# Kernel optimization log

Measured on AMD Instinct MI355X. Metric: run time of the kernel, lower is better.

## Reference

```python
import jax, jax.numpy as jnp
import numpy as np

DIM, IDIM, HEADS = 256, 64, 4
B, I, J = 1, 256, 256
EPS = 1e-5


def _sinu(seq, rot):
    inv = 1.0 / (10000.0 ** (np.arange(0, rot, 2, dtype=np.float64) / rot))
    f = np.arange(seq, dtype=np.float64)[:, None] * inv[None, :]   # [seq, rot/2]
    f = np.repeat(f, 2, axis=-1)                                   # [seq, rot]
    return (jnp.asarray(np.sin(f)[None], dtype=jnp.float32),
            jnp.asarray(np.cos(f)[None], dtype=jnp.float32))       # [1, seq, rot]


def setup_inputs() -> dict:
    key = jax.random.key(0)
    ks = jax.random.split(key, 8)
    w = DIM ** -0.5
    sin_i, cos_i = _sinu(J, IDIM)
    sin_j, cos_j = _sinu(I, IDIM)
    return {
        'x': jax.random.normal(ks[0], (B, I, J, DIM), jnp.float32),
        'sin_i': sin_i, 'cos_i': cos_i, 'sin_j': sin_j, 'cos_j': cos_j,
        'gia': jnp.ones((DIM,), jnp.float32), 'bia': jnp.zeros((DIM,), jnp.float32),
        'gib': jnp.ones((DIM,), jnp.float32), 'bib': jnp.zeros((DIM,), jnp.float32),
        'Wq_i': jax.random.normal(ks[1], (DIM, IDIM * HEADS), jnp.float32) * w,
        'Wkv_i': jax.random.normal(ks[2], (DIM, 2 * IDIM * HEADS), jnp.float32) * w,
        'Wo_i': jax.random.normal(ks[3], (IDIM * HEADS, DIM), jnp.float32) * w,
        'bo_i': jnp.zeros((DIM,), jnp.float32),
        'gja': jnp.ones((DIM,), jnp.float32), 'bja': jnp.zeros((DIM,), jnp.float32),
        'gjb': jnp.ones((DIM,), jnp.float32), 'bjb': jnp.zeros((DIM,), jnp.float32),
        'Wq_j': jax.random.normal(ks[4], (DIM, IDIM * HEADS), jnp.float32) * w,
        'Wkv_j': jax.random.normal(ks[5], (DIM, 2 * IDIM * HEADS), jnp.float32) * w,
        'Wo_j': jax.random.normal(ks[6], (IDIM * HEADS, DIM), jnp.float32) * w,
        'bo_j': jnp.zeros((DIM,), jnp.float32),
    }


def _ln(x, g, b):
    mu = jnp.mean(x, axis=-1, keepdims=True)
    var = jnp.mean((x - mu) ** 2, axis=-1, keepdims=True)
    return (x - mu) / jnp.sqrt(var + EPS) * g + b


def _rotate_every_two(x):
    x1, x2 = x[..., ::2], x[..., 1::2]
    return jnp.stack((-x2, x1), axis=-1).reshape(x.shape)


def _rope(x, sin, cos):
    # sin/cos: [1, seq, rot] -> [1, 1, seq, rot] (broadcast over heads)
    sin, cos = sin[:, None], cos[:, None]
    rd = sin.shape[-1]
    xr, xp = x[..., :rd], x[..., rd:]
    xr = xr * cos + _rotate_every_two(xr) * sin
    return jnp.concatenate((xr, xp), axis=-1)


def _attn(a, sin, cos, ga, ba, gb, bb, Wq, Wkv, Wo, bo):
    an = _ln(a, ga, ba)
    bn = _ln(a, gb, bb)  # a == b in axial use
    q = an @ Wq
    k, v = jnp.split(bn @ Wkv, 2, axis=-1)
    Bn, N = a.shape[0], a.shape[1]
    def heads(t):
        return t.reshape(Bn, N, HEADS, IDIM).transpose(0, 2, 1, 3)  # b h n d
    q, k, v = heads(q), heads(k), heads(v)
    q = _rope(q, sin, cos)
    k = _rope(k, sin, cos)
    dots = jnp.einsum('bhid,bhjd->bhij', q, k)  # scale = 1 (as in source)
    attn = jax.nn.softmax(dots, axis=-1)
    out = jnp.einsum('bhij,bhjd->bhid', attn, v)
    out = out.transpose(0, 2, 3, 1).reshape(Bn, N, IDIM * HEADS)  # 'b h i d -> b i (d h)'
    return jax.nn.elu(out @ Wo + bo)


def reference(x, sin_i, cos_i, sin_j, cos_j,
              gia, bia, gib, bib, Wq_i, Wkv_i, Wo_i, bo_i,
              gja, bja, gjb, bjb, Wq_j, Wkv_j, Wo_j, bo_j):
    b, i, j, d = x.shape
    xi = x.reshape(b * i, j, d)
    xi = _attn(xi, sin_i, cos_i, gia, bia, gib, bib, Wq_i, Wkv_i, Wo_i, bo_i)
    xi = xi.reshape(b, i, j, d)
    xj = x.transpose(0, 2, 1, 3).reshape(b * j, i, d)
    xj = _attn(xj, sin_j, cos_j, gja, bja, gjb, bjb, Wq_j, Wkv_j, Wo_j, bo_j)
    xj = xj.reshape(b, j, i, d).transpose(0, 2, 1, 3)
    return x + (xi + xj) / 2
```

## Files before the change

kernel.cpp:

```cpp
#include <hip/hip_runtime.h>
#include <math.h>

#define DIM    256
#define IDIM   64
#define HEADS  4
#define NSEQ   256
#define SEQLEN 256
#define NTOK   (NSEQ * SEQLEN)
#define EPSLN  1e-5f

typedef __attribute__((ext_vector_type(8))) short bf16x8s;
typedef __attribute__((ext_vector_type(4))) float f32x4;

union BF8 { bf16x8s v; unsigned short u[8]; };

__device__ __forceinline__ float bf2f(unsigned short u) {
    union { unsigned int i; float f; } v; v.i = ((unsigned int)u) << 16; return v.f;
}
__device__ __forceinline__ unsigned short f2bf(float f) {
    union { float f; unsigned int i; } v; v.f = f;
    unsigned int x = v.i;
    return (unsigned short)((x + 0x7fffu + ((x >> 16) & 1u)) >> 16);
}

__device__ bf16x8s g_wpk[8][8192];
__device__ float g_bias[8][256];
__device__ float g_csum[8][256];

__global__ __launch_bounds__(256) void wpack_all_kernel(
    const float* __restrict__ Wq_i, const float* __restrict__ Wkv_i,
    const float* __restrict__ Wo_i,
    const float* __restrict__ Wq_j, const float* __restrict__ Wkv_j,
    const float* __restrict__ Wo_j,
    const float* __restrict__ gia, const float* __restrict__ gib,
    const float* __restrict__ gja, const float* __restrict__ gjb)
{
    const int slot = blockIdx.y;
    const int pass = slot >> 2, m = slot & 3;
    const float* W; int ldw, col0, perm;
    const float* gam;
    if (m == 0)      { W = pass ? Wq_j  : Wq_i;  ldw = 256; col0 = 0;   perm = 0; gam = pass ? gja : gia; }
    else if (m == 1) { W = pass ? Wkv_j : Wkv_i; ldw = 512; col0 = 0;   perm = 0; gam = pass ? gjb : gib; }
    else if (m == 2) { W = pass ? Wkv_j : Wkv_i; ldw = 512; col0 = 256; perm = 0; gam = pass ? gjb : gib; }
    else             { W = pass ? Wo_j  : Wo_i;  ldw = 256; col0 = 0;   perm = 1; gam = 0; }

    const int gtile = blockIdx.x * 4 + (threadIdx.x >> 6);
    const int l = threadIdx.x & 63;
    const int nt = gtile >> 3, kt = gtile & 7;
    const int n = nt * 16 + (l & 15);
    const int k0 = kt * 32 + (l >> 4) * 8;
    BF8 o;
#pragma unroll
    for (int j = 0; j < 8; ++j) {
        int k = k0 + j;
        int src = perm ? ((k & 63) * 4 + (k >> 6)) : k;
        float wv = W[(size_t)src * ldw + col0 + n];
        if (gam) wv *= gam[k];
        o.u[j] = f2bf(wv);
    }
    g_wpk[slot][(size_t)gtile * 64 + l] = o.v;
}

__global__ __launch_bounds__(256) void bias_kernel(
    const float* __restrict__ bia, const float* __restrict__ bib,
    const float* __restrict__ bja, const float* __restrict__ bjb,
    const float* __restrict__ gia, const float* __restrict__ gib,
    const float* __restrict__ gja, const float* __restrict__ gjb,
    const float* __restrict__ Wq_i, const float* __restrict__ Wkv_i,
    const float* __restrict__ Wq_j, const float* __restrict__ Wkv_j)
{
    const int s = blockIdx.x;
    const int pass = s / 3, m = s % 3;
    const float* beta = (m == 0) ? (pass ? bja : bia) : (pass ? bjb : bib);
    const float* gam  = (m == 0) ? (pass ? gja : gia) : (pass ? gjb : gib);
    const float* W    = (m == 0) ? (pass ? Wq_j : Wq_i) : (pass ? Wkv_j : Wkv_i);
    const int ldw  = (m == 0) ? 256 : 512;
    const int col0 = (m == 2) ? 256 : 0;
    const int col  = threadIdx.x;
    float ab = 0.f, ac = 0.f;
    for (int k = 0; k < 256; ++k) {
        float wv = W[(size_t)k * ldw + col0 + col];
        ab += beta[k] * wv;
        ac += gam[k]  * wv;
    }
    g_bias[pass * 4 + m][col] = ab;
    g_csum[pass * 4 + m][col] = ac;
}

#define HLD  264
#define CLD2 261

__global__ __launch_bounds__(1024) void lnqkv_kernel(
    const float* __restrict__ x,
    const float* __restrict__ sin_t, const float* __restrict__ cos_t,
    bf16x8s* __restrict__ qo, bf16x8s* __restrict__ ko, bf16x8s* __restrict__ vo,
    int pass)
{
    __shared__ __align__(16) unsigned short smu[17024];
    unsigned short* hi = smu;
    unsigned short* lo = smu + 8448;
    float* stats = (float*)(smu + 16896);
    float* smf = (float*)smu;

    const int tid = threadIdx.x;
    const int l = tid & 63, w = tid >> 6;
    const int lr = l & 15, lk = l >> 4;
    const int t0 = blockIdx.x * 32;
    const int seq = t0 >> 8;
    const int pos0 = t0 & 255;
    const int wbase = pass * 4;

    {
        const int r  = tid >> 5;
        const int c0 = (tid & 31) * 8;
        int t = t0 + r;
        int row = (pass == 0) ? t : ((t & 255) * NSEQ + (t >> 8));
        const float4* xp = reinterpret_cast<const float4*>(&x[(size_t)row * DIM + c0]);
        float4 v0 = xp[0], v1 = xp[1];
        float vv[8] = {v0.x, v0.y, v0.z, v0.w, v1.x, v1.y, v1.z, v1.w};
        BF8 hh, ll;
#pragma unroll
        for (int j = 0; j < 8; ++j) {
            union { float f; unsigned int u; } a; a.f = vv[j];
            unsigned short h = (unsigned short)(a.u >> 16);
            hh.u[j] = h;
            ll.u[j] = f2bf(vv[j] - bf2f(h));
        }
        *reinterpret_cast<bf16x8s*>(hi + r * HLD + c0) = hh.v;
        *reinterpret_cast<bf16x8s*>(lo + r * HLD + c0) = ll.v;
    }
    __syncthreads();

    {
        const int r = tid >> 5, sub = tid & 31;
        BF8 h0, l0;
        h0.v = *(const bf16x8s*)(hi + r * HLD + sub * 8);
        l0.v = *(const bf16x8s*)(lo + r * HLD + sub * 8);
        float s1 = 0.f, s2 = 0.f;
#pragma unroll
        for (int m = 0; m < 8; ++m) {
            float v = bf2f(h0.u[m]) + bf2f(l0.u[m]);
            s1 += v; s2 += v * v;
        }
        for (int off = 1; off < 32; off <<= 1) {
            s1 += __shfl_xor(s1, off, 32);
            s2 += __shfl_xor(s2, off, 32);
        }
        float mu = s1 * (1.f / 256.f);
        float var = s2 * (1.f / 256.f) - mu * mu;
        float rstd = rsqrtf(var + EPSLN);
        if (sub == 0) { stats[r] = rstd; stats[32 + r] = mu * rstd; }
    }
    __syncthreads();

    f32x4 acc[2][3];
#pragma unroll
    for (int mp2 = 0; mp2 < 2; ++mp2)
#pragma unroll
        for (int nf = 0; nf < 3; ++nf) { f32x4 z = {0.f, 0.f, 0.f, 0.f}; acc[mp2][nf] = z; }

    const int nt0 = w * 3;

    for (int ks = 0; ks < 8; ++ks) {
        const int c0 = ks * 32 + lk * 8;
        bf16x8s b[3];
#pragma unroll
        for (int nf = 0; nf < 3; ++nf) {
            const int ntg = nt0 + nf;
            b[nf] = g_wpk[wbase + (ntg >> 4)][((size_t)((ntg & 15) * 8 + ks)) * 64 + l];
        }
#pragma unroll
        for (int mp2 = 0; mp2 < 2; ++mp2) {
            const int arow = mp2 * 16 + lr;
            const bf16x8s ahi = *(const bf16x8s*)(hi + arow * HLD + c0);
            const bf16x8s alo = *(const bf16x8s*)(lo + arow * HLD + c0);
#pragma unroll
            for (int nf = 0; nf < 3; ++nf) {
                acc[mp2][nf] = __builtin_amdgcn_mfma_f32_16x16x32_bf16(alo, b[nf], acc[mp2][nf], 0, 0, 0);
                acc[mp2][nf] = __builtin_amdgcn_mfma_f32_16x16x32_bf16(ahi, b[nf], acc[mp2][nf], 0, 0, 0);
            }
        }
    }
    __syncthreads();

    for (int c = 0; c < 3; ++c) {
#pragma unroll
        for (int nf = 0; nf < 3; ++nf) {
            int ntg = nt0 + nf;
            if ((ntg >> 4) == c) {
                int cb = (ntg & 15) * 16 + lr;
#pragma unroll
                for (int mp2 = 0; mp2 < 2; ++mp2)
#pragma unroll
                    for (int r = 0; r < 4; ++r)
                        smf[(mp2 * 16 + lk * 4 + r) * CLD2 + cb] = acc[mp2][nf][r];
            }
        }
        __syncthreads();

        if (c < 2) {
            int h = w >> 2, mt = (w >> 1) & 1, ktd = w & 1;
            int row = mt * 16 + lr;
            int pos = pos0 + row;
            int d0 = ktd * 32 + lk * 8;
            const float* src = &smf[row * CLD2 + h * 64 + d0];
            const float* bv = &g_bias[wbase + c][h * 64 + d0];
            const float* cv = &g_csum[wbase + c][h * 64 + d0];
            float rs = stats[row], mr = stats[32 + row];
            BF8 o;
#pragma unroll
            for (int p2 = 0; p2 < 4; ++p2) {
                float cs = cos_t[pos * IDIM + d0 + 2 * p2];
                float sn = sin_t[pos * IDIM + d0 + 2 * p2];
                float e  = rs * src[2 * p2]     - mr * cv[2 * p2]     + bv[2 * p2];
                float od = rs * src[2 * p2 + 1] - mr * cv[2 * p2 + 1] + bv[2 * p2 + 1];
                o.u[2 * p2]     = f2bf(e * cs - od * sn);
                o.u[2 * p2 + 1] = f2bf(od * cs + e * sn);
            }
            int sh = seq * 4 + h;
            int mtg = (pos0 >> 4) + mt;
            bf16x8s* dst = c ? ko : qo;
            dst[((size_t)sh * 32 + mtg * 2 + ktd) * 64 + l] = o.v;
        } else {
            int h = w >> 2, ntd = w & 3;
            int col = h * 64 + ntd * 16 + lr;
            float bb_ = g_bias[wbase + 2][col];
            float cc_ = g_csum[wbase + 2][col];
            BF8 o;
#pragma unroll
            for (int j = 0; j < 8; ++j) {
                int rr = lk * 8 + j;
                o.u[j] = f2bf(stats[rr] * smf[rr * CLD2 + col] - stats[32 + rr] * cc_ + bb_);
            }
            int sh = seq * 4 + h;
            int ktg = pos0 >> 5;
            vo[((size_t)sh * 32 + ktg * 4 + ntd) * 64 + l] = o.v;
        }
        __syncthreads();
    }
}

__global__ __launch_bounds__(512) void attn_kernel(
    const bf16x8s* __restrict__ qpk, const bf16x8s* __restrict__ kpk,
    const bf16x8s* __restrict__ vpk, bf16x8s* __restrict__ opk)
{
    __shared__ __align__(16) unsigned short Pus[256 * 64];
    char* Pb = (char*)Pus;
    const int tid = threadIdx.x, l = tid & 63, w = tid >> 6;
    const int lr = l & 15, lk = l >> 4;
    const int sh = blockIdx.x;
    const size_t base = (size_t)sh * 32 * 64;

    bf16x8s qf[2][2];
#pragma unroll
    for (int mf = 0; mf < 2; ++mf)
#pragma unroll
        for (int kt = 0; kt < 2; ++kt)
            qf[mf][kt] = qpk[base + ((size_t)((w * 2 + mf) * 2 + kt)) * 64 + l];

    f32x4 O[2][4];
    float mrun[2][4], lrun[2][4];
#pragma unroll
    for (int mf = 0; mf < 2; ++mf)
#pragma unroll
        for (int nf = 0; nf < 4; ++nf) { f32x4 z = {0.f, 0.f, 0.f, 0.f}; O[mf][nf] = z; }
#pragma unroll
    for (int mf = 0; mf < 2; ++mf)
#pragma unroll
        for (int r = 0; r < 4; ++r) { mrun[mf][r] = -1e30f; lrun[mf][r] = 0.f; }

    for (int ktk = 0; ktk < 4; ++ktk) {
#pragma unroll
        for (int mf = 0; mf < 2; ++mf) {
            f32x4 S[4];
#pragma unroll
            for (int nf = 0; nf < 4; ++nf) { f32x4 z = {0.f, 0.f, 0.f, 0.f}; S[nf] = z; }
#pragma unroll
            for (int ks = 0; ks < 2; ++ks) {
                bf16x8s kf[4];
#pragma unroll
                for (int nf = 0; nf < 4; ++nf)
                    kf[nf] = kpk[base + ((size_t)((ktk * 4 + nf) * 2 + ks)) * 64 + l];
#pragma unroll
                for (int nf = 0; nf < 4; ++nf)
                    S[nf] = __builtin_amdgcn_mfma_f32_16x16x32_bf16(qf[mf][ks], kf[nf], S[nf], 0, 0, 0);
            }
#pragma unroll
            for (int r = 0; r < 4; ++r) {
                float mt_ = fmaxf(fmaxf(S[0][r], S[1][r]), fmaxf(S[2][r], S[3][r]));
                for (int off = 1; off < 16; off <<= 1) mt_ = fmaxf(mt_, __shfl_xor(mt_, off, 64));
                float mnew = fmaxf(mrun[mf][r], mt_);
                float sc = __expf(mrun[mf][r] - mnew);
#pragma unroll
                for (int nf = 0; nf < 4; ++nf) O[mf][nf][r] *= sc;
                float ps = 0.f;
#pragma unroll
                for (int nf = 0; nf < 4; ++nf) {
                    float pp = __expf(S[nf][r] - mnew);
                    S[nf][r] = pp;
                    ps += pp;
                }
                for (int off = 1; off < 16; off <<= 1) ps += __shfl_xor(ps, off, 64);
                lrun[mf][r] = lrun[mf][r] * sc + ps;
                mrun[mf][r] = mnew;
            }
#pragma unroll
            for (int nf = 0; nf < 4; ++nf)
#pragma unroll
                for (int r = 0; r < 4; ++r) {
                    int row = w * 32 + mf * 16 + lk * 4 + r, col = nf * 16 + lr;
                    unsigned int byte = ((unsigned)(row * 64 + col) * 2) ^ (unsigned)((row & 7) << 4);
                    *(unsigned short*)(Pb + byte) = f2bf(S[nf][r]);
                }
        }
#pragma unroll
        for (int ks = 0; ks < 2; ++ks) {
            bf16x8s vf[4];
#pragma unroll
            for (int nf = 0; nf < 4; ++nf)
                vf[nf] = vpk[base + ((size_t)((ktk * 2 + ks) * 4 + nf)) * 64 + l];
#pragma unroll
            for (int mf = 0; mf < 2; ++mf) {
                int row = w * 32 + mf * 16 + lr;
                unsigned int byte = ((unsigned)(row * 64 + ks * 32 + lk * 8) * 2) ^ (unsigned)((row & 7) << 4);
                bf16x8s pa = *(const bf16x8s*)(Pb + byte);
#pragma unroll
                for (int nf = 0; nf < 4; ++nf)
                    O[mf][nf] = __builtin_amdgcn_mfma_f32_16x16x32_bf16(pa, vf[nf], O[mf][nf], 0, 0, 0);
            }
        }
    }

#pragma unroll
    for (int mf = 0; mf < 2; ++mf)
#pragma unroll
        for (int r = 0; r < 4; ++r) {
            float inv = 1.f / lrun[mf][r];
#pragma unroll
            for (int nf = 0; nf < 4; ++nf) {
                int row = w * 32 + mf * 16 + lk * 4 + r, col = nf * 16 + lr;
                unsigned int byte = ((unsigned)(row * 64 + col) * 2) ^ (unsigned)((row & 7) << 4);
                *(unsigned short*)(Pb + byte) = f2bf(O[mf][nf][r] * inv);
            }
        }
    const int seq = sh >> 2, h = sh & 3;
#pragma unroll
    for (int mf = 0; mf < 2; ++mf)
#pragma unroll
        for (int ktd = 0; ktd < 2; ++ktd) {
            int row = w * 32 + mf * 16 + lr;
            unsigned int byte = ((unsigned)(row * 64 + ktd * 32 + lk * 8) * 2) ^ (unsigned)((row & 7) << 4);
            bf16x8s o = *(const bf16x8s*)(Pb + byte);
            size_t mtg = (size_t)seq * 16 + w * 2 + mf;
            opk[(mtg * 8 + h * 2 + ktd) * 64 + l] = o;
        }
}

__global__ __launch_bounds__(512) void gemm_proj_kernel(
    const bf16x8s* __restrict__ A,
    const float* __restrict__ x, const float* __restrict__ bo,
    float* __restrict__ out, int pass)
{
    const int tid = threadIdx.x;
    const int l = tid & 63, w = tid >> 6;
    const int wm = w >> 1, wn = w & 1;
    const int mb = blockIdx.x;
    const bf16x8s* B = g_wpk[pass * 4 + 3];
    const int mt0 = mb * 8 + wm * 2;

#pragma unroll 1
    for (int nb = 0; nb < 2; ++nb) {
        f32x4 acc[2][4];
#pragma unroll
        for (int mf = 0; mf < 2; ++mf)
#pragma unroll
            for (int nf = 0; nf < 4; ++nf) { f32x4 z = {0.f, 0.f, 0.f, 0.f}; acc[mf][nf] = z; }

        const int nt0 = nb * 8 + wn * 4;
#pragma unroll
        for (int ks = 0; ks < 8; ++ks) {
            bf16x8s a[2], b[4];
#pragma unroll
            for (int mf = 0; mf < 2; ++mf) a[mf] = A[((size_t)(mt0 + mf) * 8 + ks) * 64 + l];
#pragma unroll
            for (int nf = 0; nf < 4; ++nf) b[nf] = B[((size_t)(nt0 + nf) * 8 + ks) * 64 + l];
#pragma unroll
            for (int mf = 0; mf < 2; ++mf)
#pragma unroll
                for (int nf = 0; nf < 4; ++nf)
                    acc[mf][nf] = __builtin_amdgcn_mfma_f32_16x16x32_bf16(a[mf], b[nf], acc[mf][nf], 0, 0, 0);
        }

#pragma unroll
        for (int mf = 0; mf < 2; ++mf)
#pragma unroll
            for (int nf = 0; nf < 4; ++nf) {
                const int col = nb * 128 + wn * 64 + nf * 16 + (l & 15);
                const float bc = bo[col];
#pragma unroll
                for (int r = 0; r < 4; ++r) {
                    int row = mb * 128 + wm * 32 + mf * 16 + (l >> 4) * 4 + r;
                    size_t prow = (pass == 0) ? (size_t)row
                                              : ((size_t)(row & 255) * NSEQ + (row >> 8));
                    size_t addr = prow * DIM + col;
                    float y = acc[mf][nf][r] + bc;
                    float e = 0.5f * (y > 0.f ? y : expm1f(y));
                    if (pass == 0) out[addr] = x[addr] + e;
                    else           out[addr] += e;
                }
            }
    }
}

extern "C" void kernel_launch(void* const* d_in, const int* in_sizes, int n_in,
                              void* d_out, int out_size, void* d_ws, size_t ws_size,
                              hipStream_t stream) {
    const float* x     = (const float*)d_in[0];
    const float* sin_i = (const float*)d_in[1];
    const float* cos_i = (const float*)d_in[2];
    const float* sin_j = (const float*)d_in[3];
    const float* cos_j = (const float*)d_in[4];
    const float* gia   = (const float*)d_in[5];
    const float* bia   = (const float*)d_in[6];
    const float* gib   = (const float*)d_in[7];
    const float* bib   = (const float*)d_in[8];
    const float* Wq_i  = (const float*)d_in[9];
    const float* Wkv_i = (const float*)d_in[10];
    const float* Wo_i  = (const float*)d_in[11];
    const float* bo_i  = (const float*)d_in[12];
    const float* gja   = (const float*)d_in[13];
    const float* bja   = (const float*)d_in[14];
    const float* gjb   = (const float*)d_in[15];
    const float* bjb   = (const float*)d_in[16];
    const float* Wq_j  = (const float*)d_in[17];
    const float* Wkv_j = (const float*)d_in[18];
    const float* Wo_j  = (const float*)d_in[19];
    const float* bo_j  = (const float*)d_in[20];

    float* out = (float*)d_out;

    char* base = (char*)d_ws;
    const size_t MB32 = 33554432;
    bf16x8s* buf0 = (bf16x8s*)(base);
    bf16x8s* buf1 = (bf16x8s*)(base + MB32);
    bf16x8s* buf2 = (bf16x8s*)(base + 2 * MB32);
    bf16x8s* buf3 = (bf16x8s*)(base + 3 * MB32);

    wpack_all_kernel<<<dim3(32, 8), 256, 0, stream>>>(
        Wq_i, Wkv_i, Wo_i, Wq_j, Wkv_j, Wo_j, gia, gib, gja, gjb);
    bias_kernel<<<6, 256, 0, stream>>>(
        bia, bib, bja, bjb, gia, gib, gja, gjb, Wq_i, Wkv_i, Wq_j, Wkv_j);

    for (int pass = 0; pass < 2; ++pass) {
        const float* sin_t = pass ? sin_j : sin_i;
        const float* cos_t = pass ? cos_j : cos_i;
        const float* bo = pass ? bo_j : bo_i;

        lnqkv_kernel<<<2048, 1024, 0, stream>>>(
            x, sin_t, cos_t, buf2, buf3, buf0, pass);
        attn_kernel<<<1024, 512, 0, stream>>>(buf2, buf3, buf0, buf1);
        gemm_proj_kernel<<<512, 512, 0, stream>>>(buf1, x, bo, out, pass);
    }
}
```

Measured before the change: 547.1 us.

## Stage all QKV chunks at once in swizzled bf16 shared memory

The epilogue of the LN+QKV projection kernel used to stage accumulators through shared memory as fp32, one 256-column chunk (Q, K, V) at a time, with two barriers per chunk. It now writes all 768 columns at once as bf16 into a larger buffer using an XOR swizzle, then runs one barrier and lets each wave handle three output groups. Q/K reads become single 16-byte vector loads. The aim is to cut barrier count and shared-memory traffic and bank conflicts. The cost is more LDS per block and an extra bf16 rounding of the raw projection before the LayerNorm mean correction, which can lose accuracy through cancellation.

```diff
diff --git a/kernel.cpp b/kernel.cpp
--- a/kernel.cpp
+++ b/kernel.cpp
@@ -88,7 +88,7 @@
 }
 
 #define HLD  264
-#define CLD2 261
+#define CW   776
 
 __global__ __launch_bounds__(1024) void lnqkv_kernel(
     const float* __restrict__ x,
@@ -96,11 +96,11 @@
     bf16x8s* __restrict__ qo, bf16x8s* __restrict__ ko, bf16x8s* __restrict__ vo,
     int pass)
 {
-    __shared__ __align__(16) unsigned short smu[17024];
+    __shared__ __align__(16) unsigned short smu[24960];
     unsigned short* hi = smu;
     unsigned short* lo = smu + 8448;
-    float* stats = (float*)(smu + 16896);
-    float* smf = (float*)smu;
+    float* stats = (float*)(smu + 24832);
+    char* cb = (char*)smu;
 
     const int tid = threadIdx.x;
     const int l = tid & 63, w = tid >> 6;
@@ -183,27 +183,32 @@
     }
     __syncthreads();
 
-    for (int c = 0; c < 3; ++c) {
-#pragma unroll
-        for (int nf = 0; nf < 3; ++nf) {
-            int ntg = nt0 + nf;
-            if ((ntg >> 4) == c) {
-                int cb = (ntg & 15) * 16 + lr;
-#pragma unroll
-                for (int mp2 = 0; mp2 < 2; ++mp2)
-#pragma unroll
-                    for (int r = 0; r < 4; ++r)
-                        smf[(mp2 * 16 + lk * 4 + r) * CLD2 + cb] = acc[mp2][nf][r];
-            }
-        }
-        __syncthreads();
-
+#pragma unroll
+    for (int nf = 0; nf < 3; ++nf) {
+        const int col = (nt0 + nf) * 16 + lr;
+#pragma unroll
+        for (int mp2 = 0; mp2 < 2; ++mp2)
+#pragma unroll
+            for (int r = 0; r < 4; ++r) {
+                int row = mp2 * 16 + lk * 4 + r;
+                unsigned byte = ((unsigned)(row * CW + col) * 2) ^ (unsigned)(((row >> 2) & 7) << 4);
+                *(unsigned short*)(cb + byte) = f2bf(acc[mp2][nf][r]);
+            }
+    }
+    __syncthreads();
+
+#pragma unroll
+    for (int p = 0; p < 3; ++p) {
+        const int g = w * 3 + p;
+        const int c = g >> 4, tt = g & 15;
         if (c < 2) {
-            int h = w >> 2, mt = (w >> 1) & 1, ktd = w & 1;
+            int h = tt >> 2, mt = (tt >> 1) & 1, ktd = tt & 1;
             int row = mt * 16 + lr;
             int pos = pos0 + row;
             int d0 = ktd * 32 + lk * 8;
-            const float* src = &smf[row * CLD2 + h * 64 + d0];
+            int col0 = c * 256 + h * 64 + d0;
+            unsigned byte = ((unsigned)(row * CW + col0) * 2) ^ (unsigned)(((row >> 2) & 7) << 4);
+            BF8 sv; sv.v = *(const bf16x8s*)(cb + byte);
             const float* bv = &g_bias[wbase + c][h * 64 + d0];
             const float* cv = &g_csum[wbase + c][h * 64 + d0];
             float rs = stats[row], mr = stats[32 + row];
@@ -212,8 +217,8 @@
             for (int p2 = 0; p2 < 4; ++p2) {
                 float cs = cos_t[pos * IDIM + d0 + 2 * p2];
                 float sn = sin_t[pos * IDIM + d0 + 2 * p2];
-                float e  = rs * src[2 * p2]     - mr * cv[2 * p2]     + bv[2 * p2];
-                float od = rs * src[2 * p2 + 1] - mr * cv[2 * p2 + 1] + bv[2 * p2 + 1];
+                float e  = rs * bf2f(sv.u[2 * p2])     - mr * cv[2 * p2]     + bv[2 * p2];
+                float od = rs * bf2f(sv.u[2 * p2 + 1]) - mr * cv[2 * p2 + 1] + bv[2 * p2 + 1];
                 o.u[2 * p2]     = f2bf(e * cs - od * sn);
                 o.u[2 * p2 + 1] = f2bf(od * cs + e * sn);
             }
@@ -222,21 +227,23 @@
             bf16x8s* dst = c ? ko : qo;
             dst[((size_t)sh * 32 + mtg * 2 + ktd) * 64 + l] = o.v;
         } else {
-            int h = w >> 2, ntd = w & 3;
-            int col = h * 64 + ntd * 16 + lr;
-            float bb_ = g_bias[wbase + 2][col];
-            float cc_ = g_csum[wbase + 2][col];
+            int h = tt >> 2, ntd = tt & 3;
+            int colr = h * 64 + ntd * 16 + lr;
+            int colv = 512 + colr;
+            float bb_ = g_bias[wbase + 2][colr];
+            float cc_ = g_csum[wbase + 2][colr];
             BF8 o;
 #pragma unroll
             for (int j = 0; j < 8; ++j) {
                 int rr = lk * 8 + j;
-                o.u[j] = f2bf(stats[rr] * smf[rr * CLD2 + col] - stats[32 + rr] * cc_ + bb_);
+                unsigned byte = ((unsigned)(rr * CW + colv) * 2) ^ (unsigned)(((rr >> 2) & 7) << 4);
+                float val = bf2f(*(const unsigned short*)(cb + byte));
+                o.u[j] = f2bf(stats[rr] * val - stats[32 + rr] * cc_ + bb_);
             }
             int sh = seq * 4 + h;
             int ktg = pos0 >> 5;
             vo[((size_t)sh * 32 + ktg * 4 + ntd) * 64 + l] = o.v;
         }
-        __syncthreads();
     }
 }
 
```

Result: slower. 578.2 us (+5.7%).
